# Kernel optimization log

Hardware: AMD Instinct MI355X
Metric: run time of the kernel (lower is better)

The kernel has to match this reference:

```python
import jax, jax.numpy as jnp
import numpy as np

B, F, V, E = 16384, 39, 100000, 16
D0, D1, D2 = 32, 32, 32

def setup_inputs() -> dict:
    key = jax.random.key(0)
    ks = jax.random.split(key, 12)
    return {
        "Xi": jax.random.randint(ks[0], (B, F, 1), 0, V),
        "Xv": jax.random.uniform(ks[1], (B, F), dtype=jnp.float32),
        "emb_tables": jax.random.normal(ks[2], (F, V, E), dtype=jnp.float32),
        "w_first": jax.random.normal(ks[3], (D0, F, E), dtype=jnp.float32),
        "w_inner": jax.random.normal(ks[4], (D0, F, E), dtype=jnp.float32),
        "lin1_W": jax.random.normal(ks[5], (D1, D0), dtype=jnp.float32) * 0.1,
        "lin1_b": jax.random.normal(ks[6], (D1,), dtype=jnp.float32) * 0.1,
        "lin2_W": jax.random.normal(ks[7], (D2, D1), dtype=jnp.float32) * 0.1,
        "lin2_b": jax.random.normal(ks[8], (D2,), dtype=jnp.float32) * 0.1,
        "last_W": jax.random.normal(ks[9], (1, D2), dtype=jnp.float32) * 0.1,
        "last_b": jax.random.normal(ks[10], (1,), dtype=jnp.float32) * 0.1,
    }

def reference(Xi, Xv, emb_tables, w_first, w_inner, lin1_W, lin1_b, lin2_W, lin2_b, last_W, last_b):
    idx = Xi[:, :, 0]                                  # [B,F]
    # per-field embedding gather, scaled by feature value
    emb = emb_tables[jnp.arange(F)[None, :], idx]      # [B,F,E]
    emb = emb * Xv[:, :, None]                         # [B,F,E]
    # first-order: nested loops over (D0, F) collapse to one einsum
    first = jnp.einsum('bfe,dfe->bd', emb, w_first)    # [B,D0]
    # inner-product second-order: (sum over fields of <emb_f, w_df>)^2
    s = jnp.einsum('bfe,dfe->bd', emb, w_inner)        # [B,D0]
    x = first + s * s
    # deep MLP (relu, no dropout/batchnorm in inference)
    x = jax.nn.relu(x @ lin1_W.T + lin1_b)
    x = jax.nn.relu(x @ lin2_W.T + lin2_b)
    x = x @ last_W.T + last_b                          # [B,1]
    return jnp.sum(x, axis=1)                          # [B]
```

## Files before the change

kernel.cpp:

```cpp
#include <hip/hip_runtime.h>


namespace {

typedef _Float16 half8 __attribute__((ext_vector_type(8)));
typedef float floatx4 __attribute__((ext_vector_type(4)));

constexpr int Bn = 16384;
constexpr int Fn = 39;
constexpr int Vn = 100000;
constexpr int En = 16;
constexpr int M = 32;
constexpr int THREADS = 512;
constexpr int AST = 648;
constexpr int KSTEPS = 20;

union SMem {
    struct {
        __align__(16) _Float16 A[M * AST];
        __align__(16) int   xi[M * Fn];
        __align__(16) float xv[M * Fn];
    } g;
    struct {
        float x[M * 69];
        float wsh[2176];
        float r1[1024];
        float r2[1024];
    } e;
};

__device__ __forceinline__ half8 cvt8s(float4 a, float4 b, float s) {
    half8 h;
    h[0] = (_Float16)(a.x * s); h[1] = (_Float16)(a.y * s);
    h[2] = (_Float16)(a.z * s); h[3] = (_Float16)(a.w * s);
    h[4] = (_Float16)(b.x * s); h[5] = (_Float16)(b.y * s);
    h[6] = (_Float16)(b.z * s); h[7] = (_Float16)(b.w * s);
    return h;
}

__device__ __forceinline__ half8 cvt8(float4 a, float4 b) {
    half8 h;
    h[0] = (_Float16)a.x; h[1] = (_Float16)a.y;
    h[2] = (_Float16)a.z; h[3] = (_Float16)a.w;
    h[4] = (_Float16)b.x; h[5] = (_Float16)b.y;
    h[6] = (_Float16)b.z; h[7] = (_Float16)b.w;
    return h;
}

__global__ __launch_bounds__(THREADS, 6) void pnn_main(
    const int* __restrict__ Xi,
    const float* __restrict__ Xv,
    const float* __restrict__ T,
    const float* __restrict__ w_first,
    const float* __restrict__ w_inner,
    const float* __restrict__ lin1_W,
    const float* __restrict__ lin1_b,
    const float* __restrict__ lin2_W,
    const float* __restrict__ lin2_b,
    const float* __restrict__ last_W,
    const float* __restrict__ last_b,
    float* __restrict__ out)
{
    __shared__ SMem sm;

    const int tid = threadIdx.x;
    const int lane = tid & 63;
    const int wv = tid >> 6;
    const int row0 = blockIdx.x * M;

    if (tid < (M * Fn) / 4) {
        reinterpret_cast<int4*>(sm.g.xi)[tid] =
            reinterpret_cast<const int4*>(Xi + (size_t)row0 * Fn)[tid];
        reinterpret_cast<float4*>(sm.g.xv)[tid] =
            reinterpret_cast<const float4*>(Xv + (size_t)row0 * Fn)[tid];
    }
    if (tid < M * 4) {
        const int r = tid >> 2, c3 = tid & 3;
        if (c3 < 3) {
            float4 z = {0.0f, 0.0f, 0.0f, 0.0f};
            *reinterpret_cast<float4*>(&sm.g.A[r * AST + 624 + c3 * 8]) = z;
        }
    }
    __syncthreads();

    for (int base = 0; base < M * Fn; base += THREADS) {
        const int i = base + tid;
        if (i < M * Fn) {
            const int r = i & 31, f = i >> 5;
            const int idx = sm.g.xi[r * Fn + f];
            const float s = sm.g.xv[r * Fn + f];
            const float4* src = reinterpret_cast<const float4*>(
                T + ((size_t)f * Vn + (size_t)idx) * En);
            const float4 q0 = src[0], q1 = src[1], q2 = src[2], q3 = src[3];
            *reinterpret_cast<half8*>(&sm.g.A[r * AST + f * 16])     = cvt8s(q0, q1, s);
            *reinterpret_cast<half8*>(&sm.g.A[r * AST + f * 16 + 8]) = cvt8s(q2, q3, s);
        }
    }
    __syncthreads();

    const int q = wv & 1;
    const int t16 = wv >> 1;
    const int m = lane & 15;
    const int g8 = (lane >> 4) * 8;
    const float* wsrc = ((t16 < 2) ? w_first : w_inner)
                        + (size_t)((t16 & 1) * 16 + m) * (Fn * En);
    const _Float16* arow = &sm.g.A[(q * 16 + m) * AST + g8];

    floatx4 acc = {0.0f, 0.0f, 0.0f, 0.0f};
#pragma unroll
    for (int t = 0; t < KSTEPS; ++t) {
        const half8 af = *reinterpret_cast<const half8*>(arow + t * 32);
        int kb = t * 32 + g8;
        kb = (kb > 616) ? 616 : kb;
        const float4 w0 = *reinterpret_cast<const float4*>(wsrc + kb);
        const float4 w1 = *reinterpret_cast<const float4*>(wsrc + kb + 4);
        acc = __builtin_amdgcn_mfma_f32_16x16x32_f16(af, cvt8(w0, w1), acc, 0, 0, 0);
    }
    __syncthreads();

    {
        const int col = t16 * 16 + m;
        const int rbase = q * 16 + (lane >> 4) * 4;
#pragma unroll
        for (int r = 0; r < 4; ++r)
            sm.e.x[(rbase + r) * 69 + col] = acc[r];
    }

    for (int i = tid; i < 2145; i += THREADS) {
        float v;
        if (i < 1024)      v = lin1_W[i];
        else if (i < 2048) v = lin2_W[i - 1024];
        else if (i < 2080) v = lin1_b[i - 2048];
        else if (i < 2112) v = lin2_b[i - 2080];
        else if (i < 2144) v = last_W[i - 2112];
        else               v = last_b[0];
        sm.e.wsh[i] = v;
    }
    __syncthreads();

    for (int p = tid; p < 1024; p += THREADS) {
        const int j = p >> 5, r = p & 31;
        const float fi = sm.e.x[r * 69 + j];
        const float s  = sm.e.x[r * 69 + 32 + j];
        sm.e.r1[j * 32 + r] = fi + s * s;
    }
    __syncthreads();

    {
        const int r = tid & 31, n0 = (tid >> 5) * 2;
        float a0 = sm.e.wsh[2048 + n0];
        float a1 = sm.e.wsh[2048 + n0 + 1];
#pragma unroll
        for (int j = 0; j < 32; ++j) {
            const float xj = sm.e.r1[j * 32 + r];
            a0 = fmaf(sm.e.wsh[n0 * 32 + j],       xj, a0);
            a1 = fmaf(sm.e.wsh[(n0 + 1) * 32 + j], xj, a1);
        }
        sm.e.r2[n0 * 32 + r]       = fmaxf(a0, 0.0f);
        sm.e.r2[(n0 + 1) * 32 + r] = fmaxf(a1, 0.0f);
    }
    __syncthreads();

    {
        const int r = tid & 31, n0 = (tid >> 5) * 2;
        float a0 = sm.e.wsh[2080 + n0];
        float a1 = sm.e.wsh[2080 + n0 + 1];
#pragma unroll
        for (int j = 0; j < 32; ++j) {
            const float xj = sm.e.r2[j * 32 + r];
            a0 = fmaf(sm.e.wsh[1024 + n0 * 32 + j],       xj, a0);
            a1 = fmaf(sm.e.wsh[1024 + (n0 + 1) * 32 + j], xj, a1);
        }
        sm.e.r1[n0 * 32 + r]       = fmaxf(a0, 0.0f);
        sm.e.r1[(n0 + 1) * 32 + r] = fmaxf(a1, 0.0f);
    }
    __syncthreads();

    if (tid < M) {
        float res = sm.e.wsh[2144];
#pragma unroll
        for (int j = 0; j < 32; ++j)
            res = fmaf(sm.e.wsh[2112 + j], sm.e.r1[j * 32 + tid], res);
        out[row0 + tid] = res;
    }
}

}

extern "C" void kernel_launch(void* const* d_in, const int* in_sizes, int n_in,
                              void* d_out, int out_size, void* d_ws, size_t ws_size,
                              hipStream_t stream) {
    (void)d_ws; (void)ws_size; (void)in_sizes; (void)n_in; (void)out_size;
    const int*   Xi      = (const int*)d_in[0];
    const float* Xv      = (const float*)d_in[1];
    const float* T       = (const float*)d_in[2];
    const float* w_first = (const float*)d_in[3];
    const float* w_inner = (const float*)d_in[4];
    const float* lin1_W  = (const float*)d_in[5];
    const float* lin1_b  = (const float*)d_in[6];
    const float* lin2_W  = (const float*)d_in[7];
    const float* lin2_b  = (const float*)d_in[8];
    const float* last_W  = (const float*)d_in[9];
    const float* last_b  = (const float*)d_in[10];
    float* out = (float*)d_out;

    dim3 grid(Bn / M);
    dim3 block(THREADS);
    hipLaunchKernelGGL(pnn_main, grid, block, 0, stream,
                       Xi, Xv, T, w_first, w_inner,
                       lin1_W, lin1_b, lin2_W, lin2_b, last_W, last_b, out);
}
```

Measured before the change: 329.9 us.

## Split into gather-stage and GEMM kernels with MFMA-fragment-ordered fp16 workspace

Splits the fused kernel in two. The first kernel gathers and scales embeddings into fp16, writing them to a global workspace already laid out in MFMA fragment order. Extra blocks of that kernel pre-convert the first-order and inner weights into fp16 fragments. The second kernel then loads A and B fragments directly with contiguous vector reads, with no per-step weight conversion, and runs the MLP epilogue. The aim is to remove redundant per-block weight conversion and raise gather parallelism through smaller blocks, at the cost of a global round trip for the activations and a second launch.

```diff
diff --git a/kernel.cpp b/kernel.cpp
--- a/kernel.cpp
+++ b/kernel.cpp
@@ -11,23 +11,10 @@
 constexpr int Vn = 100000;
 constexpr int En = 16;
 constexpr int M = 32;
-constexpr int THREADS = 512;
-constexpr int AST = 648;
-constexpr int KSTEPS = 20;
-
-union SMem {
-    struct {
-        __align__(16) _Float16 A[M * AST];
-        __align__(16) int   xi[M * Fn];
-        __align__(16) float xv[M * Fn];
-    } g;
-    struct {
-        float x[M * 69];
-        float wsh[2176];
-        float r1[1024];
-        float r2[1024];
-    } e;
-};
+constexpr int KST = 20;
+constexpr int NRT = Bn / 16;
+constexpr int WBLOCKS = 20;
+constexpr int AWS_OFF_H = 65536;
 
 __device__ __forceinline__ half8 cvt8s(float4 a, float4 b, float s) {
     half8 h;
@@ -47,12 +34,86 @@
     return h;
 }
 
-__global__ __launch_bounds__(THREADS, 6) void pnn_main(
+__global__ __launch_bounds__(256) void pnn_stage(
     const int* __restrict__ Xi,
     const float* __restrict__ Xv,
     const float* __restrict__ T,
     const float* __restrict__ w_first,
     const float* __restrict__ w_inner,
+    _Float16* __restrict__ ws)
+{
+    _Float16* __restrict__ Wws = ws;
+    _Float16* __restrict__ Aws = ws + AWS_OFF_H;
+
+    const int tid = threadIdx.x;
+
+    if (blockIdx.x >= NRT) {
+        const int slot = (blockIdx.x - NRT) * 256 + tid;
+        const int t16 = slot / (KST * 64);
+        const int rem = slot % (KST * 64);
+        const int t = rem >> 6;
+        const int lane = rem & 63;
+        const int n = t16 * 16 + (lane & 15);
+        const int kb = t * 32 + (lane >> 4) * 8;
+        half8 h = {0, 0, 0, 0, 0, 0, 0, 0};
+        if (!(t == KST - 1 && (lane >> 4) >= 2)) {
+            const float* src = ((n < 32) ? (w_first + (size_t)n * 624)
+                                         : (w_inner + (size_t)(n - 32) * 624)) + kb;
+            const float4 a = *reinterpret_cast<const float4*>(src);
+            const float4 b = *reinterpret_cast<const float4*>(src + 4);
+            h = cvt8(a, b);
+        }
+        *reinterpret_cast<half8*>(Wws + (size_t)slot * 8) = h;
+        return;
+    }
+
+    __shared__ _Float16 At[KST * 512];
+    __shared__ int   xi[624];
+    __shared__ float xv[624];
+
+    const int rt = blockIdx.x;
+    const int r0 = rt * 16;
+
+    if (tid < 156) {
+        reinterpret_cast<int4*>(xi)[tid] =
+            reinterpret_cast<const int4*>(Xi + (size_t)r0 * Fn)[tid];
+        reinterpret_cast<float4*>(xv)[tid] =
+            reinterpret_cast<const float4*>(Xv + (size_t)r0 * Fn)[tid];
+    }
+    if (tid < 32) {
+        half8 z = {0, 0, 0, 0, 0, 0, 0, 0};
+        *reinterpret_cast<half8*>(At + ((KST - 1) * 64 + 32 + tid) * 8) = z;
+    }
+    __syncthreads();
+
+    for (int i = tid; i < 624; i += 256) {
+        const int r = i & 15, f = i >> 4;
+        const int idx = xi[r * Fn + f];
+        const float s = xv[r * Fn + f];
+        const float4* src = reinterpret_cast<const float4*>(
+            T + ((size_t)f * Vn + (size_t)idx) * En);
+        const float4 q0 = src[0], q1 = src[1], q2 = src[2], q3 = src[3];
+        const int base = (((f >> 1) * 64) + (f & 1) * 32 + r) * 8;
+        *reinterpret_cast<half8*>(At + base)       = cvt8s(q0, q1, s);
+        *reinterpret_cast<half8*>(At + base + 128) = cvt8s(q2, q3, s);
+    }
+    __syncthreads();
+
+    const int4* s4 = reinterpret_cast<const int4*>(At);
+    int4* d4 = reinterpret_cast<int4*>(Aws + (size_t)rt * KST * 512);
+#pragma unroll
+    for (int j = 0; j < 5; ++j) d4[tid + j * 256] = s4[tid + j * 256];
+}
+
+struct SMemE {
+    float x[M * 69];
+    float wsh[2176];
+    float r1[1024];
+    float r2[1024];
+};
+
+__global__ __launch_bounds__(512) void pnn_gemm(
+    const _Float16* __restrict__ ws,
     const float* __restrict__ lin1_W,
     const float* __restrict__ lin1_b,
     const float* __restrict__ lin2_W,
@@ -61,72 +122,38 @@
     const float* __restrict__ last_b,
     float* __restrict__ out)
 {
-    __shared__ SMem sm;
+    __shared__ SMemE sm;
+
+    const _Float16* __restrict__ Wws = ws;
+    const _Float16* __restrict__ Aws = ws + AWS_OFF_H;
 
     const int tid = threadIdx.x;
     const int lane = tid & 63;
     const int wv = tid >> 6;
-    const int row0 = blockIdx.x * M;
-
-    if (tid < (M * Fn) / 4) {
-        reinterpret_cast<int4*>(sm.g.xi)[tid] =
-            reinterpret_cast<const int4*>(Xi + (size_t)row0 * Fn)[tid];
-        reinterpret_cast<float4*>(sm.g.xv)[tid] =
-            reinterpret_cast<const float4*>(Xv + (size_t)row0 * Fn)[tid];
-    }
-    if (tid < M * 4) {
-        const int r = tid >> 2, c3 = tid & 3;
-        if (c3 < 3) {
-            float4 z = {0.0f, 0.0f, 0.0f, 0.0f};
-            *reinterpret_cast<float4*>(&sm.g.A[r * AST + 624 + c3 * 8]) = z;
-        }
-    }
-    __syncthreads();
-
-    for (int base = 0; base < M * Fn; base += THREADS) {
-        const int i = base + tid;
-        if (i < M * Fn) {
-            const int r = i & 31, f = i >> 5;
-            const int idx = sm.g.xi[r * Fn + f];
-            const float s = sm.g.xv[r * Fn + f];
-            const float4* src = reinterpret_cast<const float4*>(
-                T + ((size_t)f * Vn + (size_t)idx) * En);
-            const float4 q0 = src[0], q1 = src[1], q2 = src[2], q3 = src[3];
-            *reinterpret_cast<half8*>(&sm.g.A[r * AST + f * 16])     = cvt8s(q0, q1, s);
-            *reinterpret_cast<half8*>(&sm.g.A[r * AST + f * 16 + 8]) = cvt8s(q2, q3, s);
-        }
-    }
-    __syncthreads();
-
     const int q = wv & 1;
     const int t16 = wv >> 1;
-    const int m = lane & 15;
-    const int g8 = (lane >> 4) * 8;
-    const float* wsrc = ((t16 < 2) ? w_first : w_inner)
-                        + (size_t)((t16 & 1) * 16 + m) * (Fn * En);
-    const _Float16* arow = &sm.g.A[(q * 16 + m) * AST + g8];
+    const int row0 = blockIdx.x * M;
+
+    const _Float16* aptr = Aws + ((size_t)(blockIdx.x * 2 + q) * KST) * 512 + lane * 8;
+    const _Float16* bptr = Wws + ((size_t)t16 * KST) * 512 + lane * 8;
 
     floatx4 acc = {0.0f, 0.0f, 0.0f, 0.0f};
 #pragma unroll
-    for (int t = 0; t < KSTEPS; ++t) {
-        const half8 af = *reinterpret_cast<const half8*>(arow + t * 32);
-        int kb = t * 32 + g8;
-        kb = (kb > 616) ? 616 : kb;
-        const float4 w0 = *reinterpret_cast<const float4*>(wsrc + kb);
-        const float4 w1 = *reinterpret_cast<const float4*>(wsrc + kb + 4);
-        acc = __builtin_amdgcn_mfma_f32_16x16x32_f16(af, cvt8(w0, w1), acc, 0, 0, 0);
-    }
-    __syncthreads();
+    for (int t = 0; t < KST; ++t) {
+        const half8 af = *reinterpret_cast<const half8*>(aptr + t * 512);
+        const half8 bf = *reinterpret_cast<const half8*>(bptr + t * 512);
+        acc = __builtin_amdgcn_mfma_f32_16x16x32_f16(af, bf, acc, 0, 0, 0);
+    }
 
     {
-        const int col = t16 * 16 + m;
+        const int col = t16 * 16 + (lane & 15);
         const int rbase = q * 16 + (lane >> 4) * 4;
 #pragma unroll
         for (int r = 0; r < 4; ++r)
-            sm.e.x[(rbase + r) * 69 + col] = acc[r];
-    }
-
-    for (int i = tid; i < 2145; i += THREADS) {
+            sm.x[(rbase + r) * 69 + col] = acc[r];
+    }
+
+    for (int i = tid; i < 2145; i += 512) {
         float v;
         if (i < 1024)      v = lin1_W[i];
         else if (i < 2048) v = lin2_W[i - 1024];
@@ -134,53 +161,53 @@
         else if (i < 2112) v = lin2_b[i - 2080];
         else if (i < 2144) v = last_W[i - 2112];
         else               v = last_b[0];
-        sm.e.wsh[i] = v;
-    }
-    __syncthreads();
-
-    for (int p = tid; p < 1024; p += THREADS) {
+        sm.wsh[i] = v;
+    }
+    __syncthreads();
+
+    for (int p = tid; p < 1024; p += 512) {
         const int j = p >> 5, r = p & 31;
-        const float fi = sm.e.x[r * 69 + j];
-        const float s  = sm.e.x[r * 69 + 32 + j];
-        sm.e.r1[j * 32 + r] = fi + s * s;
+        const float fi = sm.x[r * 69 + j];
+        const float s  = sm.x[r * 69 + 32 + j];
+        sm.r1[j * 32 + r] = fi + s * s;
     }
     __syncthreads();
 
     {
         const int r = tid & 31, n0 = (tid >> 5) * 2;
-        float a0 = sm.e.wsh[2048 + n0];
-        float a1 = sm.e.wsh[2048 + n0 + 1];
+        float a0 = sm.wsh[2048 + n0];
+        float a1 = sm.wsh[2048 + n0 + 1];
 #pragma unroll
         for (int j = 0; j < 32; ++j) {
-            const float xj = sm.e.r1[j * 32 + r];
-            a0 = fmaf(sm.e.wsh[n0 * 32 + j],       xj, a0);
-            a1 = fmaf(sm.e.wsh[(n0 + 1) * 32 + j], xj, a1);
+            const float xj = sm.r1[j * 32 + r];
+            a0 = fmaf(sm.wsh[n0 * 32 + j],       xj, a0);
+            a1 = fmaf(sm.wsh[(n0 + 1) * 32 + j], xj, a1);
         }
-        sm.e.r2[n0 * 32 + r]       = fmaxf(a0, 0.0f);
-        sm.e.r2[(n0 + 1) * 32 + r] = fmaxf(a1, 0.0f);
+        sm.r2[n0 * 32 + r]       = fmaxf(a0, 0.0f);
+        sm.r2[(n0 + 1) * 32 + r] = fmaxf(a1, 0.0f);
     }
     __syncthreads();
 
     {
         const int r = tid & 31, n0 = (tid >> 5) * 2;
-        float a0 = sm.e.wsh[2080 + n0];
-        float a1 = sm.e.wsh[2080 + n0 + 1];
+        float a0 = sm.wsh[2080 + n0];
+        float a1 = sm.wsh[2080 + n0 + 1];
 #pragma unroll
         for (int j = 0; j < 32; ++j) {
-            const float xj = sm.e.r2[j * 32 + r];
-            a0 = fmaf(sm.e.wsh[1024 + n0 * 32 + j],       xj, a0);
-            a1 = fmaf(sm.e.wsh[1024 + (n0 + 1) * 32 + j], xj, a1);
+            const float xj = sm.r2[j * 32 + r];
+            a0 = fmaf(sm.wsh[1024 + n0 * 32 + j],       xj, a0);
+            a1 = fmaf(sm.wsh[1024 + (n0 + 1) * 32 + j], xj, a1);
         }
-        sm.e.r1[n0 * 32 + r]       = fmaxf(a0, 0.0f);
-        sm.e.r1[(n0 + 1) * 32 + r] = fmaxf(a1, 0.0f);
+        sm.r1[n0 * 32 + r]       = fmaxf(a0, 0.0f);
+        sm.r1[(n0 + 1) * 32 + r] = fmaxf(a1, 0.0f);
     }
     __syncthreads();
 
     if (tid < M) {
-        float res = sm.e.wsh[2144];
+        float res = sm.wsh[2144];
 #pragma unroll
         for (int j = 0; j < 32; ++j)
-            res = fmaf(sm.e.wsh[2112 + j], sm.e.r1[j * 32 + tid], res);
+            res = fmaf(sm.wsh[2112 + j], sm.r1[j * 32 + tid], res);
         out[row0 + tid] = res;
     }
 }
@@ -190,7 +217,7 @@
 extern "C" void kernel_launch(void* const* d_in, const int* in_sizes, int n_in,
                               void* d_out, int out_size, void* d_ws, size_t ws_size,
                               hipStream_t stream) {
-    (void)d_ws; (void)ws_size; (void)in_sizes; (void)n_in; (void)out_size;
+    (void)in_sizes; (void)n_in; (void)out_size; (void)ws_size;
     const int*   Xi      = (const int*)d_in[0];
     const float* Xv      = (const float*)d_in[1];
     const float* T       = (const float*)d_in[2];
@@ -203,10 +230,10 @@
     const float* last_W  = (const float*)d_in[9];
     const float* last_b  = (const float*)d_in[10];
     float* out = (float*)d_out;
-
-    dim3 grid(Bn / M);
-    dim3 block(THREADS);
-    hipLaunchKernelGGL(pnn_main, grid, block, 0, stream,
-                       Xi, Xv, T, w_first, w_inner,
-                       lin1_W, lin1_b, lin2_W, lin2_b, last_W, last_b, out);
-}
+    _Float16* ws = (_Float16*)d_ws;
+
+    hipLaunchKernelGGL(pnn_stage, dim3(NRT + WBLOCKS), dim3(256), 0, stream,
+                       Xi, Xv, T, w_first, w_inner, ws);
+    hipLaunchKernelGGL(pnn_gemm, dim3(Bn / M), dim3(512), 0, stream,
+                       ws, lin1_W, lin1_b, lin2_W, lin2_b, last_W, last_b, out);
+}
```

Result: no change. 330.4 us (+0.2%).

## Split embedding gather into 16B-per-thread loads and store A in MFMA-fragment layout

Applied to the files above, without the earlier changes.

The gather now has each thread fetch a single 16-byte quarter of an embedding row with a nontemporal load, batching five loads before converting and storing. This raises memory-level parallelism compared with one thread loading a whole 64-byte row. The A tile is written directly in MFMA fragment order, so each lane reads a contiguous half8 per k-step, avoiding the padded row stride and possible bank conflicts. The union grows because the epilogue region is now placed after the tile, which may affect LDS occupancy.

```diff
diff --git a/kernel.cpp b/kernel.cpp
--- a/kernel.cpp
+++ b/kernel.cpp
@@ -4,24 +4,27 @@
 namespace {
 
 typedef _Float16 half8 __attribute__((ext_vector_type(8)));
+typedef _Float16 half4 __attribute__((ext_vector_type(4)));
 typedef float floatx4 __attribute__((ext_vector_type(4)));
+typedef float f32x4 __attribute__((ext_vector_type(4)));
 
 constexpr int Bn = 16384;
 constexpr int Fn = 39;
 constexpr int Vn = 100000;
 constexpr int En = 16;
 constexpr int M = 32;
+constexpr int KST = 20;
 constexpr int THREADS = 512;
-constexpr int AST = 648;
-constexpr int KSTEPS = 20;
+constexpr int TILE_H = KST * 512;
 
 union SMem {
     struct {
-        __align__(16) _Float16 A[M * AST];
+        __align__(16) _Float16 At[2 * TILE_H];
         __align__(16) int   xi[M * Fn];
         __align__(16) float xv[M * Fn];
     } g;
     struct {
+        _Float16 At_pad[2 * TILE_H];
         float x[M * 69];
         float wsh[2176];
         float r1[1024];
@@ -29,12 +32,12 @@
     } e;
 };
 
-__device__ __forceinline__ half8 cvt8s(float4 a, float4 b, float s) {
-    half8 h;
-    h[0] = (_Float16)(a.x * s); h[1] = (_Float16)(a.y * s);
-    h[2] = (_Float16)(a.z * s); h[3] = (_Float16)(a.w * s);
-    h[4] = (_Float16)(b.x * s); h[5] = (_Float16)(b.y * s);
-    h[6] = (_Float16)(b.z * s); h[7] = (_Float16)(b.w * s);
+__device__ __forceinline__ half4 cvt4s(f32x4 a, float s) {
+    half4 h;
+    h[0] = (_Float16)(a[0] * s);
+    h[1] = (_Float16)(a[1] * s);
+    h[2] = (_Float16)(a[2] * s);
+    h[3] = (_Float16)(a[3] * s);
     return h;
 }
 
@@ -47,7 +50,7 @@
     return h;
 }
 
-__global__ __launch_bounds__(THREADS, 6) void pnn_main(
+__global__ __launch_bounds__(THREADS, 6) void pnn_fused(
     const int* __restrict__ Xi,
     const float* __restrict__ Xv,
     const float* __restrict__ T,
@@ -68,49 +71,64 @@
     const int wv = tid >> 6;
     const int row0 = blockIdx.x * M;
 
-    if (tid < (M * Fn) / 4) {
+    if (tid < 312) {
         reinterpret_cast<int4*>(sm.g.xi)[tid] =
             reinterpret_cast<const int4*>(Xi + (size_t)row0 * Fn)[tid];
         reinterpret_cast<float4*>(sm.g.xv)[tid] =
             reinterpret_cast<const float4*>(Xv + (size_t)row0 * Fn)[tid];
     }
-    if (tid < M * 4) {
-        const int r = tid >> 2, c3 = tid & 3;
-        if (c3 < 3) {
-            float4 z = {0.0f, 0.0f, 0.0f, 0.0f};
-            *reinterpret_cast<float4*>(&sm.g.A[r * AST + 624 + c3 * 8]) = z;
-        }
-    }
-    __syncthreads();
-
-    for (int base = 0; base < M * Fn; base += THREADS) {
-        const int i = base + tid;
-        if (i < M * Fn) {
-            const int r = i & 31, f = i >> 5;
-            const int idx = sm.g.xi[r * Fn + f];
-            const float s = sm.g.xv[r * Fn + f];
-            const float4* src = reinterpret_cast<const float4*>(
-                T + ((size_t)f * Vn + (size_t)idx) * En);
-            const float4 q0 = src[0], q1 = src[1], q2 = src[2], q3 = src[3];
-            *reinterpret_cast<half8*>(&sm.g.A[r * AST + f * 16])     = cvt8s(q0, q1, s);
-            *reinterpret_cast<half8*>(&sm.g.A[r * AST + f * 16 + 8]) = cvt8s(q2, q3, s);
+    if (tid < 64) {
+        const int t = tid >> 5, s = tid & 31;
+        half8 z = {0, 0, 0, 0, 0, 0, 0, 0};
+        *reinterpret_cast<half8*>(
+            sm.g.At + t * TILE_H + (KST - 1) * 512 + 256 + s * 8) = z;
+    }
+    __syncthreads();
+
+#pragma unroll
+    for (int half_b = 0; half_b < 2; ++half_b) {
+        f32x4 v[5];
+        float s[5];
+        int   slot[5];
+        bool  ok[5];
+#pragma unroll
+        for (int it = 0; it < 5; ++it) {
+            const int i = tid + (half_b * 5 + it) * THREADS;
+            ok[it] = (i < M * Fn * 4);
+            if (ok[it]) {
+                const int j = i >> 2, c = i & 3;
+                const int r = j & 31, f = j >> 5;
+                const int idx = sm.g.xi[r * Fn + f];
+                s[it] = sm.g.xv[r * Fn + f];
+                const f32x4* src = reinterpret_cast<const f32x4*>(
+                    T + ((size_t)f * Vn + (size_t)idx) * En + c * 4);
+                v[it] = __builtin_nontemporal_load(src);
+                slot[it] = (r >> 4) * TILE_H
+                           + (f >> 1) * 512 + (f & 1) * 256 + (r & 15) * 8
+                           + (c >> 1) * 128 + (c & 1) * 4;
+            }
+        }
+#pragma unroll
+        for (int it = 0; it < 5; ++it) {
+            if (ok[it])
+                *reinterpret_cast<half4*>(sm.g.At + slot[it]) = cvt4s(v[it], s[it]);
         }
     }
     __syncthreads();
 
     const int q = wv & 1;
     const int t16 = wv >> 1;
-    const int m = lane & 15;
-    const int g8 = (lane >> 4) * 8;
-    const float* wsrc = ((t16 < 2) ? w_first : w_inner)
-                        + (size_t)((t16 & 1) * 16 + m) * (Fn * En);
-    const _Float16* arow = &sm.g.A[(q * 16 + m) * AST + g8];
+    const int n = t16 * 16 + (lane & 15);
+    const int koff = (lane >> 4) * 8;
+    const float* wsrc = ((n < 32) ? (w_first + (size_t)n * 624)
+                                  : (w_inner + (size_t)(n - 32) * 624));
+    const _Float16* aptr = sm.g.At + q * TILE_H + lane * 8;
 
     floatx4 acc = {0.0f, 0.0f, 0.0f, 0.0f};
 #pragma unroll
-    for (int t = 0; t < KSTEPS; ++t) {
-        const half8 af = *reinterpret_cast<const half8*>(arow + t * 32);
-        int kb = t * 32 + g8;
+    for (int t = 0; t < KST; ++t) {
+        const half8 af = *reinterpret_cast<const half8*>(aptr + t * 512);
+        int kb = t * 32 + koff;
         kb = (kb > 616) ? 616 : kb;
         const float4 w0 = *reinterpret_cast<const float4*>(wsrc + kb);
         const float4 w1 = *reinterpret_cast<const float4*>(wsrc + kb + 4);
@@ -119,7 +137,7 @@
     __syncthreads();
 
     {
-        const int col = t16 * 16 + m;
+        const int col = t16 * 16 + (lane & 15);
         const int rbase = q * 16 + (lane >> 4) * 4;
 #pragma unroll
         for (int r = 0; r < 4; ++r)
@@ -141,8 +159,8 @@
     for (int p = tid; p < 1024; p += THREADS) {
         const int j = p >> 5, r = p & 31;
         const float fi = sm.e.x[r * 69 + j];
-        const float s  = sm.e.x[r * 69 + 32 + j];
-        sm.e.r1[j * 32 + r] = fi + s * s;
+        const float sq = sm.e.x[r * 69 + 32 + j];
+        sm.e.r1[j * 32 + r] = fi + sq * sq;
     }
     __syncthreads();
 
@@ -190,7 +208,7 @@
 extern "C" void kernel_launch(void* const* d_in, const int* in_sizes, int n_in,
                               void* d_out, int out_size, void* d_ws, size_t ws_size,
                               hipStream_t stream) {
-    (void)d_ws; (void)ws_size; (void)in_sizes; (void)n_in; (void)out_size;
+    (void)in_sizes; (void)n_in; (void)out_size; (void)d_ws; (void)ws_size;
     const int*   Xi      = (const int*)d_in[0];
     const float* Xv      = (const float*)d_in[1];
     const float* T       = (const float*)d_in[2];
@@ -204,9 +222,7 @@
     const float* last_b  = (const float*)d_in[10];
     float* out = (float*)d_out;
 
-    dim3 grid(Bn / M);
-    dim3 block(THREADS);
-    hipLaunchKernelGGL(pnn_main, grid, block, 0, stream,
+    hipLaunchKernelGGL(pnn_fused, dim3(Bn / M), dim3(THREADS), 0, stream,
                        Xi, Xv, T, w_first, w_inner,
                        lin1_W, lin1_b, lin2_W, lin2_b, last_W, last_b, out);
 }
```

After: 324.3 us. No clear change (-1.7%).
